# Kernel tuning notes

Hardware: AMD Instinct MI355X
Metric: run time of the kernel (lower is better)

The kernel has to match this reference:

```python
import jax, jax.numpy as jnp
import numpy as np

OMEGA = 10.0
SIGMA = 10.0
HID = 256
IN_DIM = 3
OUT_DIM = 3


def gabor(x, W, b):
    # torch.nn.Linear: lin = x @ W.T + b
    lin = x @ W.T + b
    # exp(1j*omega*lin - (sigma*lin)**2).real == cos(omega*lin) * exp(-(sigma*lin)**2)
    return jnp.cos(OMEGA * lin) * jnp.exp(-jnp.square(SIGMA * lin))


def _linear_init(key, out_dim, in_dim):
    kw, kb = jax.random.split(key)
    bound = 1.0 / np.sqrt(in_dim)
    W = jax.random.uniform(kw, (out_dim, in_dim), jnp.float32, -bound, bound)
    b = jax.random.uniform(kb, (out_dim,), jnp.float32, -bound, bound)
    return W, b


def setup_inputs() -> dict:
    key = jax.random.key(0)
    keys = jax.random.split(key, 7)
    N = 262144
    x = jax.random.uniform(keys[0], (N, IN_DIM), jnp.float32)
    W0, b0 = _linear_init(keys[1], HID, IN_DIM)
    W1, b1 = _linear_init(keys[2], HID, HID)
    W2, b2 = _linear_init(keys[3], HID, HID)
    W3, b3 = _linear_init(keys[4], HID, HID + IN_DIM)  # skip-concat layer
    W4, b4 = _linear_init(keys[5], HID, HID)
    Wf, bf = _linear_init(keys[6], OUT_DIM, HID)
    return {"x": x, "W0": W0, "b0": b0, "W1": W1, "b1": b1, "W2": W2,
            "b2": b2, "W3": W3, "b3": b3, "W4": W4, "b4": b4,
            "Wf": Wf, "bf": bf}


def reference(x, W0, b0, W1, b1, W2, b2, W3, b3, W4, b4, Wf, bf):
    x_in = x
    h = gabor(x, W0, b0)          # net[0]
    h = gabor(h, W1, b1)          # net[1]
    h = gabor(h, W2, b2)          # net[2]
    h = jnp.concatenate([h, x_in], axis=-1)  # skip before net[3]
    h = gabor(h, W3, b3)          # net[3]
    h = gabor(h, W4, b4)          # net[4]
    return h @ Wf.T + bf          # final linear
```

## Files before the change

kernel.cpp:

```cpp
#include <hip/hip_runtime.h>

typedef _Float16 f16x8 __attribute__((ext_vector_type(8)));
typedef _Float16 f16x4 __attribute__((ext_vector_type(4)));
typedef float    f32x4 __attribute__((ext_vector_type(4)));

#define BN    64
#define KPAD  288
#define ROWB  (KPAD * 2)
#define WELE  270336

__device__ __forceinline__ int swz(int row, int colb) {
  int c = (colb < 512) ? (colb ^ ((row & 7) << 4)) : colb;
  return row * ROWB + c;
}

__device__ __forceinline__ float gabor_f(float lin) {
  float a = 10.f * lin;
  return __cosf(a) * __expf(-a * a);
}

template <int KS>
__device__ __forceinline__ void mfma_layer(const char* __restrict__ inb,
                                           char* __restrict__ outb,
                                           const _Float16* __restrict__ Wh,
                                           const _Float16* __restrict__ Wl,
                                           const float* __restrict__ bias,
                                           int lane, int wid, int phase) {
  const int r = lane & 15;
  const int g = lane >> 4;
  const int n0 = wid * 32;
  f32x4 acc[2][4];
#pragma unroll
  for (int i = 0; i < 2; i++)
#pragma unroll
    for (int j = 0; j < 4; j++) {
      f32x4 z = {0.f, 0.f, 0.f, 0.f};
      acc[i][j] = z;
    }

#pragma unroll
  for (int kk = 0; kk < KS; kk++) {
    int kkr = kk + phase;
    if (kkr >= KS) kkr -= KS;

    const int wof = (wid * KS + kkr) * 1024 + lane * 8;
    f16x8 a0 = *(const f16x8*)(Wh + wof);
    f16x8 a1 = *(const f16x8*)(Wh + wof + 512);
    f16x8 c0 = *(const f16x8*)(Wl + wof);
    f16x8 c1 = *(const f16x8*)(Wl + wof + 512);

    const int kb = kkr * 32 + g * 8;
    f16x8 b0 = *(const f16x8*)(inb + swz(0 * 16 + r, kb * 2));
    f16x8 b1 = *(const f16x8*)(inb + swz(1 * 16 + r, kb * 2));
    f16x8 b2 = *(const f16x8*)(inb + swz(2 * 16 + r, kb * 2));
    f16x8 b3 = *(const f16x8*)(inb + swz(3 * 16 + r, kb * 2));

    acc[0][0] = __builtin_amdgcn_mfma_f32_16x16x32_f16(a0, b0, acc[0][0], 0, 0, 0);
    acc[0][1] = __builtin_amdgcn_mfma_f32_16x16x32_f16(a0, b1, acc[0][1], 0, 0, 0);
    acc[0][2] = __builtin_amdgcn_mfma_f32_16x16x32_f16(a0, b2, acc[0][2], 0, 0, 0);
    acc[0][3] = __builtin_amdgcn_mfma_f32_16x16x32_f16(a0, b3, acc[0][3], 0, 0, 0);
    acc[1][0] = __builtin_amdgcn_mfma_f32_16x16x32_f16(a1, b0, acc[1][0], 0, 0, 0);
    acc[1][1] = __builtin_amdgcn_mfma_f32_16x16x32_f16(a1, b1, acc[1][1], 0, 0, 0);
    acc[1][2] = __builtin_amdgcn_mfma_f32_16x16x32_f16(a1, b2, acc[1][2], 0, 0, 0);
    acc[1][3] = __builtin_amdgcn_mfma_f32_16x16x32_f16(a1, b3, acc[1][3], 0, 0, 0);
    acc[0][0] = __builtin_amdgcn_mfma_f32_16x16x32_f16(c0, b0, acc[0][0], 0, 0, 0);
    acc[0][1] = __builtin_amdgcn_mfma_f32_16x16x32_f16(c0, b1, acc[0][1], 0, 0, 0);
    acc[0][2] = __builtin_amdgcn_mfma_f32_16x16x32_f16(c0, b2, acc[0][2], 0, 0, 0);
    acc[0][3] = __builtin_amdgcn_mfma_f32_16x16x32_f16(c0, b3, acc[0][3], 0, 0, 0);
    acc[1][0] = __builtin_amdgcn_mfma_f32_16x16x32_f16(c1, b0, acc[1][0], 0, 0, 0);
    acc[1][1] = __builtin_amdgcn_mfma_f32_16x16x32_f16(c1, b1, acc[1][1], 0, 0, 0);
    acc[1][2] = __builtin_amdgcn_mfma_f32_16x16x32_f16(c1, b2, acc[1][2], 0, 0, 0);
    acc[1][3] = __builtin_amdgcn_mfma_f32_16x16x32_f16(c1, b3, acc[1][3], 0, 0, 0);
  }

#pragma unroll
  for (int i = 0; i < 2; i++) {
    const f32x4 bv = *(const f32x4*)(bias + n0 + i * 16 + g * 4);
#pragma unroll
    for (int j = 0; j < 4; j++) {
      f16x4 hv;
#pragma unroll
      for (int e = 0; e < 4; e++)
        hv[e] = (_Float16)gabor_f(acc[i][j][e] + bv[e]);
      *(f16x4*)(outb + swz(j * 16 + r, (n0 + i * 16 + g * 4) * 2)) = hv;
    }
  }
}

extern "C" __global__ void __launch_bounds__(512, 4)
inr_fused(const float* __restrict__ x, const float* __restrict__ W0,
          const float* __restrict__ b0, const float* __restrict__ b1,
          const float* __restrict__ b2, const float* __restrict__ b3,
          const float* __restrict__ b4, const float* __restrict__ Wf,
          const float* __restrict__ bf, const _Float16* __restrict__ wsh,
          float* __restrict__ out, int npts) {
  extern __shared__ char smem[];
  char* bufA = smem;
  char* bufB = smem + BN * ROWB;

  const _Float16* w1h = wsh;
  const _Float16* w2h = wsh + 65536;
  const _Float16* w4h = wsh + 131072;
  const _Float16* w3p = wsh + 196608;
  const _Float16* w1l = wsh + WELE;
  const _Float16* w2l = wsh + WELE + 65536;
  const _Float16* w4l = wsh + WELE + 131072;
  const _Float16* w3l = wsh + WELE + 196608;

  const int tid   = threadIdx.x;
  const int pbase = blockIdx.x * BN;
  const int phase = blockIdx.x & 7;

  {
    const int p = tid >> 3;
    const int q = tid & 7;
    const int gp = pbase + p;
    float x0 = 0.f, x1 = 0.f, x2 = 0.f;
    if (gp < npts) {
      x0 = x[(size_t)gp * 3 + 0];
      x1 = x[(size_t)gp * 3 + 1];
      x2 = x[(size_t)gp * 3 + 2];
    }
#pragma unroll
    for (int ub = 0; ub < 32; ub += 8) {
      const int u0 = q * 32 + ub;
      f16x8 hv;
#pragma unroll
      for (int e = 0; e < 8; e++) {
        const int u = u0 + e;
        float lin = fmaf(x0, W0[u * 3 + 0],
                    fmaf(x1, W0[u * 3 + 1],
                    fmaf(x2, W0[u * 3 + 2], b0[u])));
        hv[e] = (_Float16)gabor_f(lin);
      }
      *(f16x8*)(bufA + swz(p, u0 * 2)) = hv;
    }
    if (q < 4) {
      f16x8 xv = {(_Float16)0.f, (_Float16)0.f, (_Float16)0.f, (_Float16)0.f,
                  (_Float16)0.f, (_Float16)0.f, (_Float16)0.f, (_Float16)0.f};
      if (q == 0) { xv[0] = (_Float16)x0; xv[1] = (_Float16)x1; xv[2] = (_Float16)x2; }
      *(f16x8*)(bufA + swz(p, (256 + q * 8) * 2)) = xv;
    }
  }
  __syncthreads();

  const int lane = tid & 63;
  const int wid  = tid >> 6;

  mfma_layer<8>(bufA, bufB, w1h, w1l, b1, lane, wid, phase);
  __syncthreads();
  mfma_layer<8>(bufB, bufA, w2h, w2l, b2, lane, wid, phase);
  __syncthreads();
  mfma_layer<9>(bufA, bufB, w3p, w3l, b3, lane, wid, phase);
  __syncthreads();
  mfma_layer<8>(bufB, bufA, w4h, w4l, b4, lane, wid, phase);
  __syncthreads();

  if (tid < BN * 3) {
    const int p = tid / 3;
    const int o = tid - p * 3;
    const int gp = pbase + p;
    if (gp < npts) {
      float a0 = bf[o], a1 = 0.f, a2 = 0.f, a3 = 0.f;
#pragma unroll 4
      for (int k = 0; k < 256; k += 8) {
        f16x8 hv = *(const f16x8*)(bufA + swz(p, k * 2));
        f32x4 wa = *(const f32x4*)(Wf + o * 256 + k);
        f32x4 wb = *(const f32x4*)(Wf + o * 256 + k + 4);
        a0 = fmaf((float)hv[0], wa[0], a0);
        a1 = fmaf((float)hv[1], wa[1], a1);
        a2 = fmaf((float)hv[2], wa[2], a2);
        a3 = fmaf((float)hv[3], wa[3], a3);
        a0 = fmaf((float)hv[4], wb[0], a0);
        a1 = fmaf((float)hv[5], wb[1], a1);
        a2 = fmaf((float)hv[6], wb[2], a2);
        a3 = fmaf((float)hv[7], wb[3], a3);
      }
      out[(size_t)gp * 3 + o] = (a0 + a1) + (a2 + a3);
    }
  }
}

extern "C" __global__ void conv_w(const float* __restrict__ W1,
                                  const float* __restrict__ W2,
                                  const float* __restrict__ W4,
                                  const float* __restrict__ W3,
                                  _Float16* __restrict__ wsh) {
  int idx = blockIdx.x * blockDim.x + threadIdx.x;
  if (idx >= WELE) return;

  int base, KS;
  const float* src = nullptr;
  int ldk = 256, kmax = 256;
  if (idx < 65536)       { base = 0;      KS = 8; src = W1; }
  else if (idx < 131072) { base = 65536;  KS = 8; src = W2; }
  else if (idx < 196608) { base = 131072; KS = 8; src = W4; }
  else                   { base = 196608; KS = 9; src = W3; ldk = 259; kmax = 259; }

  const int t    = idx - base;
  const int e    = t & 7;
  const int lane = (t >> 3) & 63;
  const int i    = (t >> 9) & 1;
  const int rem  = t >> 10;
  const int kk   = rem % KS;
  const int slice = rem / KS;

  const int unit = slice * 32 + i * 16 + (lane & 15);
  const int k    = kk * 32 + (lane >> 4) * 8 + e;

  const float w = (k < kmax) ? src[(size_t)unit * ldk + k] : 0.f;
  const _Float16 hi = (_Float16)w;
  const _Float16 lo = (_Float16)(w - (float)hi);
  wsh[idx] = hi;
  wsh[idx + WELE] = lo;
}

extern "C" void kernel_launch(void* const* d_in, const int* in_sizes, int n_in,
                              void* d_out, int out_size, void* d_ws, size_t ws_size,
                              hipStream_t stream) {
  const float* x  = (const float*)d_in[0];
  const float* W0 = (const float*)d_in[1];
  const float* b0 = (const float*)d_in[2];
  const float* W1 = (const float*)d_in[3];
  const float* b1 = (const float*)d_in[4];
  const float* W2 = (const float*)d_in[5];
  const float* b2 = (const float*)d_in[6];
  const float* W3 = (const float*)d_in[7];
  const float* b3 = (const float*)d_in[8];
  const float* W4 = (const float*)d_in[9];
  const float* b4 = (const float*)d_in[10];
  const float* Wf = (const float*)d_in[11];
  const float* bf = (const float*)d_in[12];
  float* out      = (float*)d_out;
  _Float16* wsh   = (_Float16*)d_ws;

  const int npts = in_sizes[0] / 3;

  conv_w<<<(WELE + 511) / 512, 512, 0, stream>>>(W1, W2, W4, W3, wsh);

  const int nblk = (npts + BN - 1) / BN;
  inr_fused<<<nblk, 512, 2 * BN * ROWB, stream>>>(x, W0, b0, b1, b2, b3, b4,
                                                  Wf, bf, wsh, out, npts);
}
```

Measured before the change: 401.3 us.

## Precompute LDS offsets, drop phase rotation, parallelize final layer, relax launch bounds

The per-block K-phase rotation is removed, and LDS B-operand addresses are precomputed once per layer with immediate offsets, which cuts address arithmetic in the inner MFMA loop. The final 256-to-3 linear layer now spreads each point across 8 threads that compute all three outputs and reduce with xor shuffles, replacing 192 threads that each did a full serial dot product. Launch bounds drop from 4 to 3 blocks per CU, giving the compiler more registers at the cost of occupancy. Removing the phase rotation may bring back contention on weight cache lines across blocks.

```diff
diff --git a/kernel.cpp b/kernel.cpp
--- a/kernel.cpp
+++ b/kernel.cpp
@@ -25,10 +25,20 @@
                                            const _Float16* __restrict__ Wh,
                                            const _Float16* __restrict__ Wl,
                                            const float* __restrict__ bias,
-                                           int lane, int wid, int phase) {
+                                           int lane, int wid) {
   const int r = lane & 15;
   const int g = lane >> 4;
   const int n0 = wid * 32;
+  const int x = (r & 7) << 4;
+
+  int boff[4][2];
+#pragma unroll
+  for (int j = 0; j < 4; j++) {
+    const int row = j * 16 + r;
+    boff[j][0] = row * ROWB + ((g * 16) ^ x);
+    boff[j][1] = row * ROWB + ((64 + g * 16) ^ x);
+  }
+
   f32x4 acc[2][4];
 #pragma unroll
   for (int i = 0; i < 2; i++)
@@ -38,22 +48,30 @@
       acc[i][j] = z;
     }
 
+  const int wbase = (wid * KS) * 1024 + lane * 8;
+
 #pragma unroll
   for (int kk = 0; kk < KS; kk++) {
-    int kkr = kk + phase;
-    if (kkr >= KS) kkr -= KS;
-
-    const int wof = (wid * KS + kkr) * 1024 + lane * 8;
+    const int wof = wbase + kk * 1024;
     f16x8 a0 = *(const f16x8*)(Wh + wof);
     f16x8 a1 = *(const f16x8*)(Wh + wof + 512);
     f16x8 c0 = *(const f16x8*)(Wl + wof);
     f16x8 c1 = *(const f16x8*)(Wl + wof + 512);
 
-    const int kb = kkr * 32 + g * 8;
-    f16x8 b0 = *(const f16x8*)(inb + swz(0 * 16 + r, kb * 2));
-    f16x8 b1 = *(const f16x8*)(inb + swz(1 * 16 + r, kb * 2));
-    f16x8 b2 = *(const f16x8*)(inb + swz(2 * 16 + r, kb * 2));
-    f16x8 b3 = *(const f16x8*)(inb + swz(3 * 16 + r, kb * 2));
+    f16x8 b0, b1, b2, b3;
+    if (kk < 8) {
+      const int imm = (kk >> 1) * 128;
+      b0 = *(const f16x8*)(inb + boff[0][kk & 1] + imm);
+      b1 = *(const f16x8*)(inb + boff[1][kk & 1] + imm);
+      b2 = *(const f16x8*)(inb + boff[2][kk & 1] + imm);
+      b3 = *(const f16x8*)(inb + boff[3][kk & 1] + imm);
+    } else {
+      const int lin0 = r * ROWB + 512 + g * 16;
+      b0 = *(const f16x8*)(inb + lin0);
+      b1 = *(const f16x8*)(inb + lin0 + 16 * ROWB);
+      b2 = *(const f16x8*)(inb + lin0 + 32 * ROWB);
+      b3 = *(const f16x8*)(inb + lin0 + 48 * ROWB);
+    }
 
     acc[0][0] = __builtin_amdgcn_mfma_f32_16x16x32_f16(a0, b0, acc[0][0], 0, 0, 0);
     acc[0][1] = __builtin_amdgcn_mfma_f32_16x16x32_f16(a0, b1, acc[0][1], 0, 0, 0);
@@ -87,7 +105,7 @@
   }
 }
 
-extern "C" __global__ void __launch_bounds__(512, 4)
+extern "C" __global__ void __launch_bounds__(512, 3)
 inr_fused(const float* __restrict__ x, const float* __restrict__ W0,
           const float* __restrict__ b0, const float* __restrict__ b1,
           const float* __restrict__ b2, const float* __restrict__ b3,
@@ -109,7 +127,6 @@
 
   const int tid   = threadIdx.x;
   const int pbase = blockIdx.x * BN;
-  const int phase = blockIdx.x & 7;
 
   {
     const int p = tid >> 3;
@@ -147,36 +164,50 @@
   const int lane = tid & 63;
   const int wid  = tid >> 6;
 
-  mfma_layer<8>(bufA, bufB, w1h, w1l, b1, lane, wid, phase);
-  __syncthreads();
-  mfma_layer<8>(bufB, bufA, w2h, w2l, b2, lane, wid, phase);
-  __syncthreads();
-  mfma_layer<9>(bufA, bufB, w3p, w3l, b3, lane, wid, phase);
-  __syncthreads();
-  mfma_layer<8>(bufB, bufA, w4h, w4l, b4, lane, wid, phase);
-  __syncthreads();
-
-  if (tid < BN * 3) {
-    const int p = tid / 3;
-    const int o = tid - p * 3;
+  mfma_layer<8>(bufA, bufB, w1h, w1l, b1, lane, wid);
+  __syncthreads();
+  mfma_layer<8>(bufB, bufA, w2h, w2l, b2, lane, wid);
+  __syncthreads();
+  mfma_layer<9>(bufA, bufB, w3p, w3l, b3, lane, wid);
+  __syncthreads();
+  mfma_layer<8>(bufB, bufA, w4h, w4l, b4, lane, wid);
+  __syncthreads();
+
+  {
+    const int p = tid >> 3;
+    const int q = tid & 7;
     const int gp = pbase + p;
-    if (gp < npts) {
-      float a0 = bf[o], a1 = 0.f, a2 = 0.f, a3 = 0.f;
-#pragma unroll 4
-      for (int k = 0; k < 256; k += 8) {
-        f16x8 hv = *(const f16x8*)(bufA + swz(p, k * 2));
-        f32x4 wa = *(const f32x4*)(Wf + o * 256 + k);
-        f32x4 wb = *(const f32x4*)(Wf + o * 256 + k + 4);
-        a0 = fmaf((float)hv[0], wa[0], a0);
-        a1 = fmaf((float)hv[1], wa[1], a1);
-        a2 = fmaf((float)hv[2], wa[2], a2);
-        a3 = fmaf((float)hv[3], wa[3], a3);
-        a0 = fmaf((float)hv[4], wb[0], a0);
-        a1 = fmaf((float)hv[5], wb[1], a1);
-        a2 = fmaf((float)hv[6], wb[2], a2);
-        a3 = fmaf((float)hv[7], wb[3], a3);
+    const int xo = (p & 7) << 4;
+    const char* rowp = bufA + p * ROWB;
+    float s0 = 0.f, s1 = 0.f, s2 = 0.f;
+#pragma unroll
+    for (int i8 = 0; i8 < 4; i8++) {
+      const int ke = q * 32 + i8 * 8;
+      f16x8 hv = *(const f16x8*)(rowp + ((ke * 2) ^ xo));
+      const f32x4 w0a = *(const f32x4*)(Wf + 0 * 256 + ke);
+      const f32x4 w0b = *(const f32x4*)(Wf + 0 * 256 + ke + 4);
+      const f32x4 w1a = *(const f32x4*)(Wf + 1 * 256 + ke);
+      const f32x4 w1b = *(const f32x4*)(Wf + 1 * 256 + ke + 4);
+      const f32x4 w2a = *(const f32x4*)(Wf + 2 * 256 + ke);
+      const f32x4 w2b = *(const f32x4*)(Wf + 2 * 256 + ke + 4);
+#pragma unroll
+      for (int e = 0; e < 4; e++) {
+        const float ha = (float)hv[e];
+        const float hb = (float)hv[e + 4];
+        s0 = fmaf(ha, w0a[e], fmaf(hb, w0b[e], s0));
+        s1 = fmaf(ha, w1a[e], fmaf(hb, w1b[e], s1));
+        s2 = fmaf(ha, w2a[e], fmaf(hb, w2b[e], s2));
       }
-      out[(size_t)gp * 3 + o] = (a0 + a1) + (a2 + a3);
+    }
+#pragma unroll
+    for (int m = 1; m < 8; m <<= 1) {
+      s0 += __shfl_xor(s0, m, 64);
+      s1 += __shfl_xor(s1, m, 64);
+      s2 += __shfl_xor(s2, m, 64);
+    }
+    if (gp < npts && q < 3) {
+      const float v = (q == 0) ? (s0 + bf[0]) : ((q == 1) ? (s1 + bf[1]) : (s2 + bf[2]));
+      out[(size_t)gp * 3 + q] = v;
     }
   }
 }
```

New measurement: 415.3 us. 1.03x slower.
